# Performance work log

Measured on AMD Instinct MI355X. Metric: run time of the kernel, lower is better.

## Reference

```python
import jax, jax.numpy as jnp
import numpy as np

N_ATOMS = 10000
N_EDGES = 250000
F_DIM = 128
N_RBF = 20
CUTOFF = 5.0
N_INT = 3
EPS = 1e-8


def setup_inputs() -> dict:
    key = jax.random.key(0)
    ks = jax.random.split(key, 16)
    inp = {}
    inp["atomic_numbers"] = jax.random.randint(ks[0], (N_ATOMS,), 1, 101)
    # positions in a 5 Angstrom box so many pairs lie inside the cutoff
    inp["R"] = jax.random.uniform(ks[1], (N_ATOMS, 3), dtype=jnp.float32) * 5.0
    idx_i = jnp.sort(jax.random.randint(ks[2], (N_EDGES,), 0, N_ATOMS))
    # ensure idx_j != idx_i so d_ij > 0
    idx_j = (idx_i + 1 + jax.random.randint(ks[3], (N_EDGES,), 0, N_ATOMS - 1)) % N_ATOMS
    inp["idx_i"] = idx_i
    inp["idx_j"] = idx_j
    inp["offsets"] = jnp.zeros((N_EDGES, 3), dtype=jnp.float32)

    def w(k, shape):
        fan_in = shape[-2]
        return jax.random.normal(k, shape, dtype=jnp.float32) / np.sqrt(fan_in).astype(np.float32)

    inp["emb"] = jax.random.normal(ks[4], (101, F_DIM), dtype=jnp.float32)
    inp["filt_W"] = w(ks[5], (N_RBF, 3 * F_DIM))
    inp["filt_b"] = jax.random.normal(ks[6], (3 * F_DIM,), dtype=jnp.float32) * 0.01
    inp["int_W1"] = w(ks[7], (N_INT, F_DIM, F_DIM))
    inp["int_b1"] = jnp.zeros((N_INT, 1, F_DIM), dtype=jnp.float32)
    inp["int_W2"] = w(ks[8], (N_INT, F_DIM, 3 * F_DIM))
    inp["int_b2"] = jnp.zeros((N_INT, 1, 3 * F_DIM), dtype=jnp.float32)
    inp["mix_Wmu"] = w(ks[9], (N_INT, F_DIM, 2 * F_DIM))
    inp["mix_W1"] = w(ks[10], (N_INT, 2 * F_DIM, F_DIM))
    inp["mix_b1"] = jnp.zeros((N_INT, 1, F_DIM), dtype=jnp.float32)
    inp["mix_W2"] = w(ks[11], (N_INT, F_DIM, 3 * F_DIM))
    inp["mix_b2"] = jnp.zeros((N_INT, 1, 3 * F_DIM), dtype=jnp.float32)
    return inp


def painn_forward(atomic_numbers, idx_i, idx_j, R, offsets, emb, filt_W, filt_b,
                  int_W1, int_b1, int_W2, int_b2,
                  mix_Wmu, mix_W1, mix_b1, mix_W2, mix_b2):
    n_atoms = atomic_numbers.shape[0]
    # geometry
    r_ij = R[idx_j] - R[idx_i] + offsets                      # [E,3]
    d_ij = jnp.linalg.norm(r_ij, axis=1, keepdims=True)       # [E,1]
    dir_ij = r_ij / d_ij                                      # [E,3]
    # Gaussian radial basis + cosine cutoff (schnetpack defaults)
    centers = jnp.linspace(0.0, CUTOFF, N_RBF, dtype=jnp.float32)
    coeff = -0.5 / (centers[1] - centers[0]) ** 2
    phi = jnp.exp(coeff * (d_ij[..., None] - centers) ** 2)   # [E,1,N_RBF]
    fcut = 0.5 * (jnp.cos(d_ij * (jnp.pi / CUTOFF)) + 1.0) * (d_ij < CUTOFF)  # [E,1]
    Wij = (phi @ filt_W + filt_b) * fcut[..., None]           # [E,1,3F] (shared filters)

    q = emb[atomic_numbers][:, None, :]                       # [N,1,F]
    mu = jnp.zeros((n_atoms, 3, F_DIM), dtype=q.dtype)        # [N,3,F]

    for i in range(N_INT):
        # ---- interaction (equivariant message passing) ----
        x = jax.nn.silu(q @ int_W1[i] + int_b1[i]) @ int_W2[i] + int_b2[i]  # [N,1,3F]
        xj = x[idx_j]                                          # [E,1,3F]
        muj = mu[idx_j]                                        # [E,3,F]
        xw = Wij * xj                                          # [E,1,3F]
        dq, dmuR, dmumu = jnp.split(xw, 3, axis=-1)            # each [E,1,F]
        dq = jax.ops.segment_sum(dq, idx_i, num_segments=n_atoms)          # [N,1,F]
        dmu = dmuR * dir_ij[..., None] + dmumu * muj           # [E,3,F]
        dmu = jax.ops.segment_sum(dmu, idx_i, num_segments=n_atoms)        # [N,3,F]
        q = q + dq
        mu = mu + dmu
        # ---- mixing (intra-atomic) ----
        mu_mix = mu @ mix_Wmu[i]                               # [N,3,2F]
        mu_V, mu_W = jnp.split(mu_mix, 2, axis=-1)             # [N,3,F] each
        mu_Vn = jnp.sqrt(jnp.sum(mu_V ** 2, axis=-2, keepdims=True) + EPS)  # [N,1,F]
        ctx = jnp.concatenate([q, mu_Vn], axis=-1)             # [N,1,2F]
        xm = jax.nn.silu(ctx @ mix_W1[i] + mix_b1[i]) @ mix_W2[i] + mix_b2[i]  # [N,1,3F]
        dq_intra, dmu_intra, dqmu_intra = jnp.split(xm, 3, axis=-1)
        dmu_intra = dmu_intra * mu_W                           # [N,3,F]
        dqmu_intra = dqmu_intra * jnp.sum(mu_V * mu_W, axis=1, keepdims=True)  # [N,1,F]
        q = q + dq_intra + dqmu_intra
        mu = mu + dmu_intra

    return q.squeeze(1), mu                                    # [N,F], [N,3,F]


def reference(atomic_numbers, R, idx_i, idx_j, offsets, emb, filt_W, filt_b,
              int_W1, int_b1, int_W2, int_b2,
              mix_Wmu, mix_W1, mix_b1, mix_W2, mix_b2):
    return painn_forward(atomic_numbers, idx_i, idx_j, R, offsets, emb, filt_W, filt_b,
                         int_W1, int_b1, int_W2, int_b2,
                         mix_Wmu, mix_W1, mix_b1, mix_W2, mix_b2)
```

## Files before the change

### kernel.cpp

```cpp
#include <hip/hip_runtime.h>
#include <math.h>

#define NA 10000
#define NE 250000
#define FD 128
#define NRBF 20
#define RCUT 5.0f

typedef _Float16 h16;
typedef __attribute__((ext_vector_type(8))) _Float16 half8;
typedef __attribute__((ext_vector_type(2))) _Float16 half2v;
typedef __attribute__((ext_vector_type(4))) float f32x4;

static __device__ __forceinline__ half8 f32x8_to_h8(const float* p) {
    float4 a = *(const float4*)p;
    float4 b = *(const float4*)(p + 4);
    half8 r;
    r[0] = (h16)a.x; r[1] = (h16)a.y; r[2] = (h16)a.z; r[3] = (h16)a.w;
    r[4] = (h16)b.x; r[5] = (h16)b.y; r[6] = (h16)b.z; r[7] = (h16)b.w;
    return r;
}
static __device__ __forceinline__ float silu(float v) {
    return v / (1.f + expf(-v));
}

__global__ void csr_kernel(const int* __restrict__ idx_i, int* __restrict__ row_start,
                           int* __restrict__ cnt)
{
    int n = blockIdx.x * 256 + threadIdx.x;
    if (n > NA) return;
    int lo = 0, hi = NE;
    while (lo < hi) {
        int mid = (lo + hi) >> 1;
        if (idx_i[mid] < n) lo = mid + 1; else hi = mid;
    }
    row_start[n] = lo;
    if (n < NA) cnt[n] = 0;
}

__global__ __launch_bounds__(256) void setup_kernel(
    const float* __restrict__ R, const int* __restrict__ idx_i,
    const int* __restrict__ idx_j, const float* __restrict__ offsets,
    float* __restrict__ dir, h16* __restrict__ ph, int* __restrict__ jdx,
    const int* __restrict__ row_start, int* __restrict__ cnt,
    const float* __restrict__ int_W1, const float* __restrict__ int_W2,
    const float* __restrict__ mix_Wmu, const float* __restrict__ mix_W1,
    const float* __restrict__ mix_W2,
    h16* __restrict__ W1t, h16* __restrict__ W2t, h16* __restrict__ WmuT,
    h16* __restrict__ mW1t, h16* __restrict__ mW2t,
    const float* __restrict__ filt_W, const float* __restrict__ filt_b,
    h16* __restrict__ fwt)
{
    const int b = blockIdx.x;
    if (b < 977) {
        int e = b * 256 + threadIdx.x;
        if (e >= NE) return;
        int i = idx_i[e], j = idx_j[e];
        float rx = R[j * 3 + 0] - R[i * 3 + 0] + offsets[e * 3 + 0];
        float ry = R[j * 3 + 1] - R[i * 3 + 1] + offsets[e * 3 + 1];
        float rz = R[j * 3 + 2] - R[i * 3 + 2] + offsets[e * 3 + 2];
        float d = sqrtf(rx * rx + ry * ry + rz * rz);
        if (d >= RCUT) return;
        float inv = 1.f / d;
        float fcut = 0.5f * (cosf(d * (3.14159265358979323846f / RCUT)) + 1.f);
        int pos = atomicAdd(&cnt[i], 1);
        int s = row_start[i] + pos;
        *(float4*)&dir[(size_t)s * 4] = make_float4(rx * inv, ry * inv, rz * inv, 0.f);
        jdx[s] = j;
        h16* pp = ph + (size_t)s * 32;
        const float delta = RCUT / 19.f;
        const float coeff = -0.5f / (delta * delta);
#pragma unroll
        for (int r = 0; r < NRBF; ++r) {
            float dc = d - (float)r * delta;
            pp[r] = (h16)(expf(coeff * dc * dc) * fcut);
        }
        pp[20] = (h16)fcut;
#pragma unroll
        for (int r = 21; r < 32; ++r) pp[r] = (h16)0.f;
    } else {
        int idx = (b - 977) * 256 + threadIdx.x;
        if (idx < 49152) {
            int bt = idx >> 14, rem = idx & 16383;
            int nn = rem >> 7, kk = rem & 127;
            W1t[idx] = (h16)int_W1[(size_t)bt * 16384 + kk * 128 + nn];
        } else if ((idx -= 49152) < 147456) {
            int bt = idx / 49152, rem = idx - bt * 49152;
            int nn = rem >> 7, kk = rem & 127;
            W2t[idx] = (h16)int_W2[(size_t)bt * 49152 + kk * 384 + nn];
        } else if ((idx -= 147456) < 98304) {
            int bt = idx >> 15, rem = idx & 32767;
            int nn = rem >> 7, kk = rem & 127;
            WmuT[idx] = (h16)mix_Wmu[(size_t)bt * 32768 + kk * 256 + nn];
        } else if ((idx -= 98304) < 98304) {
            int bt = idx >> 15, rem = idx & 32767;
            int nn = rem >> 8, kk = rem & 255;
            mW1t[idx] = (h16)mix_W1[(size_t)bt * 32768 + kk * 128 + nn];
        } else if ((idx -= 98304) < 147456) {
            int bt = idx / 49152, rem = idx - bt * 49152;
            int nn = rem >> 7, kk = rem & 127;
            mW2t[idx] = (h16)mix_W2[(size_t)bt * 49152 + kk * 384 + nn];
        } else if ((idx -= 147456) < 12288) {
            int nn = idx >> 5, kk = idx & 31;
            float v = 0.f;
            if (kk < 20) v = filt_W[kk * 384 + nn];
            else if (kk == 20) v = filt_b[nn];
            fwt[idx] = (h16)v;
        }
    }
}

__global__ __launch_bounds__(256) void intmlp0_kernel(
    const int* __restrict__ Z, const float* __restrict__ emb, float* __restrict__ q,
    const h16* __restrict__ W1t, const float* __restrict__ b1,
    const h16* __restrict__ W2t, const float* __restrict__ b2, h16* __restrict__ x16)
{
    __shared__ h16 Hs[16 * 136];
    const int tid = threadIdx.x;
    const int wave = tid >> 6, lane = tid & 63;
    const int ar = lane & 15, kg = lane >> 4;
    const size_t row0 = (size_t)blockIdx.x * 16;

    {
        int a = tid >> 4, f0 = (tid & 15) * 8;
        const float* src = emb + (size_t)Z[row0 + a] * 128 + f0;
        float4 v0 = *(const float4*)src;
        float4 v1 = *(const float4*)(src + 4);
        *(float4*)&q[(row0 + a) * 128 + f0] = v0;
        *(float4*)&q[(row0 + a) * 128 + f0 + 4] = v1;
    }
    const int zr = Z[row0 + ar];
    f32x4 a1[2] = {};
    for (int ks = 0; ks < 128; ks += 32) {
        int k = ks + kg * 8;
        half8 af = f32x8_to_h8(emb + (size_t)zr * 128 + k);
#pragma unroll
        for (int tt = 0; tt < 2; ++tt) {
            int t = wave * 2 + tt;
            half8 bf = *(const half8*)&W1t[(size_t)(t * 16 + ar) * 128 + k];
            a1[tt] = __builtin_amdgcn_mfma_f32_16x16x32_f16(af, bf, a1[tt], 0, 0, 0);
        }
    }
#pragma unroll
    for (int tt = 0; tt < 2; ++tt) {
        int col = (wave * 2 + tt) * 16 + ar;
        float bb = b1[col];
#pragma unroll
        for (int r = 0; r < 4; ++r)
            Hs[(kg * 4 + r) * 136 + col] = (h16)silu(a1[tt][r] + bb);
    }
    __syncthreads();
    f32x4 a2[6] = {};
    for (int ks = 0; ks < 128; ks += 32) {
        int k = ks + kg * 8;
        half8 af = *(const half8*)&Hs[ar * 136 + k];
#pragma unroll
        for (int tt = 0; tt < 6; ++tt) {
            int t = wave * 6 + tt;
            half8 bf = *(const half8*)&W2t[(size_t)(t * 16 + ar) * 128 + k];
            a2[tt] = __builtin_amdgcn_mfma_f32_16x16x32_f16(af, bf, a2[tt], 0, 0, 0);
        }
    }
#pragma unroll
    for (int tt = 0; tt < 6; ++tt) {
        int col = (wave * 6 + tt) * 16 + ar;
        float bb = b2[col];
#pragma unroll
        for (int r = 0; r < 4; ++r)
            x16[(row0 + kg * 4 + r) * 384 + col] = (h16)(a2[tt][r] + bb);
    }
}

template<bool HAS_MU>
__global__ __launch_bounds__(128) void edge_kernel(
    const float* __restrict__ dir, const h16* __restrict__ ph,
    const h16* __restrict__ fwt,
    const int* __restrict__ row_start, const int* __restrict__ cnt,
    const int* __restrict__ jdx,
    const h16* __restrict__ x16, const h16* __restrict__ mu16p,
    const float* __restrict__ mup, float* __restrict__ mun,
    h16* __restrict__ mu16n, float* __restrict__ q)
{
    const int n = blockIdx.x, f = threadIdx.x;
    half2v fa[12], fb[12], fc[12];
    {
        const half8* pa = (const half8*)(fwt + (size_t)f * 32);
        const half8* pb = (const half8*)(fwt + (size_t)(128 + f) * 32);
#pragma unroll
        for (int r = 0; r < 3; ++r) {
            *(half8*)&fa[r * 4] = pa[r];
            *(half8*)&fb[r * 4] = pb[r];
        }
        if (HAS_MU) {
            const half8* pc = (const half8*)(fwt + (size_t)(256 + f) * 32);
#pragma unroll
            for (int r = 0; r < 3; ++r)
                *(half8*)&fc[r * 4] = pc[r];
        }
    }
    float accq = 0.f, am0 = 0.f, am1 = 0.f, am2 = 0.f;
    const int e0 = row_start[n], e1 = e0 + cnt[n];
    for (int e = e0; e < e1; ++e) {
        half2v pr[12];
        const h16* pb8 = ph + (size_t)e * 32;
        *(half8*)&pr[0] = *(const half8*)pb8;
        *(half8*)&pr[4] = *(const half8*)(pb8 + 8);
        *(half8*)&pr[8] = *(const half8*)(pb8 + 16);
        half2v A0 = {(h16)0.f, (h16)0.f}, A1 = A0, A2 = A0;
#pragma unroll
        for (int r = 0; r < 11; ++r) {
            A0 = pr[r] * fa[r] + A0;
            A1 = pr[r] * fb[r] + A1;
            if (HAS_MU) A2 = pr[r] * fc[r] + A2;
        }
        float w0 = (float)A0[0] + (float)A0[1];
        float w1 = (float)A1[0] + (float)A1[1];
        int j = jdx[e];
        float4 g = *(const float4*)&dir[(size_t)e * 4];
        const h16* xb = x16 + (size_t)j * 384;
        float x0 = (float)xb[f], x1 = (float)xb[128 + f];
        accq = fmaf(w0, x0, accq);
        float xw1 = w1 * x1;
        if (HAS_MU) {
            float w2 = (float)A2[0] + (float)A2[1];
            float x2 = (float)xb[256 + f];
            float xw2 = w2 * x2;
            const h16* mb = mu16p + (size_t)j * 384;
            am0 += xw1 * g.x + xw2 * (float)mb[f];
            am1 += xw1 * g.y + xw2 * (float)mb[128 + f];
            am2 += xw1 * g.z + xw2 * (float)mb[256 + f];
        } else {
            am0 = fmaf(xw1, g.x, am0);
            am1 = fmaf(xw1, g.y, am1);
            am2 = fmaf(xw1, g.z, am2);
        }
    }
    q[(size_t)n * FD + f] += accq;
    size_t b = (size_t)n * 384;
    float m0 = (HAS_MU ? mup[b + f] : 0.f) + am0;
    float m1 = (HAS_MU ? mup[b + 128 + f] : 0.f) + am1;
    float m2 = (HAS_MU ? mup[b + 256 + f] : 0.f) + am2;
    mun[b + f] = m0; mun[b + 128 + f] = m1; mun[b + 256 + f] = m2;
    mu16n[b + f] = (h16)m0; mu16n[b + 128 + f] = (h16)m1; mu16n[b + 256 + f] = (h16)m2;
}

__global__ __launch_bounds__(256) void mixint_kernel(
    const h16* __restrict__ mu16n, const h16* __restrict__ WmuT,
    const h16* __restrict__ W1t, const float* __restrict__ b1,
    const h16* __restrict__ W2t, const float* __restrict__ b2,
    float* __restrict__ q, float* __restrict__ mu, h16* __restrict__ mu16w,
    const h16* __restrict__ nW1t, const float* __restrict__ nb1,
    const h16* __restrict__ nW2t, const float* __restrict__ nb2,
    h16* __restrict__ x16)
{
    __shared__ h16 MM[48 * 264];
    __shared__ h16 CT[16 * 264];
    __shared__ h16 Hs[16 * 136];
    const int tid = threadIdx.x;
    const int wave = tid >> 6, lane = tid & 63;
    const int ar = lane & 15, kg = lane >> 4;
    const size_t row0 = (size_t)blockIdx.x * 16;

    {
        f32x4 acc[3][4] = {};
        int aloc[3], dloc[3];
#pragma unroll
        for (int rt = 0; rt < 3; ++rt) {
            int rr = rt * 16 + ar;
            aloc[rt] = rr / 3;
            dloc[rt] = rr - 3 * aloc[rt];
        }
        for (int ks = 0; ks < 128; ks += 32) {
            int k = ks + kg * 8;
            half8 afr[3];
#pragma unroll
            for (int rt = 0; rt < 3; ++rt)
                afr[rt] = *(const half8*)&mu16n[(row0 + aloc[rt]) * 384 + dloc[rt] * 128 + k];
#pragma unroll
            for (int ct = 0; ct < 4; ++ct) {
                int cc = wave * 4 + ct;
                half8 bf = *(const half8*)&WmuT[(size_t)(cc * 16 + ar) * 128 + k];
#pragma unroll
                for (int rt = 0; rt < 3; ++rt)
                    acc[rt][ct] = __builtin_amdgcn_mfma_f32_16x16x32_f16(afr[rt], bf, acc[rt][ct], 0, 0, 0);
            }
        }
#pragma unroll
        for (int rt = 0; rt < 3; ++rt)
#pragma unroll
            for (int ct = 0; ct < 4; ++ct) {
                int col = (wave * 4 + ct) * 16 + ar;
#pragma unroll
                for (int r = 0; r < 4; ++r)
                    MM[(rt * 16 + kg * 4 + r) * 264 + col] = (h16)acc[rt][ct][r];
            }
    }
    __syncthreads();

    {
        int a = tid >> 4, fi = (tid & 15) * 8;
        const float* qp = q + (row0 + a) * 128 + fi;
        float4 q0 = *(const float4*)qp;
        float4 q1 = *(const float4*)(qp + 4);
        float qv[8] = {q0.x, q0.y, q0.z, q0.w, q1.x, q1.y, q1.z, q1.w};
#pragma unroll
        for (int jj = 0; jj < 8; ++jj) {
            int ff = fi + jj;
            float v0 = (float)MM[(a * 3 + 0) * 264 + ff];
            float v1 = (float)MM[(a * 3 + 1) * 264 + ff];
            float v2 = (float)MM[(a * 3 + 2) * 264 + ff];
            CT[a * 264 + 128 + ff] = (h16)sqrtf(v0 * v0 + v1 * v1 + v2 * v2 + 1e-8f);
            CT[a * 264 + ff] = (h16)qv[jj];
        }
    }
    __syncthreads();

    {
        f32x4 a1[2] = {};
        for (int ks = 0; ks < 256; ks += 32) {
            int k = ks + kg * 8;
            half8 af = *(const half8*)&CT[ar * 264 + k];
#pragma unroll
            for (int tt = 0; tt < 2; ++tt) {
                int t = wave * 2 + tt;
                half8 bf = *(const half8*)&W1t[(size_t)(t * 16 + ar) * 256 + k];
                a1[tt] = __builtin_amdgcn_mfma_f32_16x16x32_f16(af, bf, a1[tt], 0, 0, 0);
            }
        }
#pragma unroll
        for (int tt = 0; tt < 2; ++tt) {
            int col = (wave * 2 + tt) * 16 + ar;
            float bb = b1[col];
#pragma unroll
            for (int r = 0; r < 4; ++r)
                Hs[(kg * 4 + r) * 136 + col] = (h16)silu(a1[tt][r] + bb);
        }
    }
    __syncthreads();

    f32x4 aq[2] = {}, am[2] = {}, ag[2] = {};
    for (int ks = 0; ks < 128; ks += 32) {
        int k = ks + kg * 8;
        half8 af = *(const half8*)&Hs[ar * 136 + k];
#pragma unroll
        for (int p = 0; p < 2; ++p) {
            int t = wave * 2 + p;
            half8 bq = *(const half8*)&W2t[(size_t)(t * 16 + ar) * 128 + k];
            aq[p] = __builtin_amdgcn_mfma_f32_16x16x32_f16(af, bq, aq[p], 0, 0, 0);
            half8 bm = *(const half8*)&W2t[(size_t)((8 + t) * 16 + ar) * 128 + k];
            am[p] = __builtin_amdgcn_mfma_f32_16x16x32_f16(af, bm, am[p], 0, 0, 0);
            half8 bg = *(const half8*)&W2t[(size_t)((16 + t) * 16 + ar) * 128 + k];
            ag[p] = __builtin_amdgcn_mfma_f32_16x16x32_f16(af, bg, ag[p], 0, 0, 0);
        }
    }

#pragma unroll
    for (int p = 0; p < 2; ++p) {
        int f = (wave * 2 + p) * 16 + ar;
        float bdq = b2[f], bdm = b2[128 + f], bdg = b2[256 + f];
#pragma unroll
        for (int r = 0; r < 4; ++r) {
            int aL = kg * 4 + r;
            size_t n = row0 + aL;
            float dq  = aq[p][r] + bdq;
            float dm  = am[p][r] + bdm;
            float dqm = ag[p][r] + bdg;
            float v0 = (float)MM[(aL * 3 + 0) * 264 + f], w0 = (float)MM[(aL * 3 + 0) * 264 + 128 + f];
            float v1 = (float)MM[(aL * 3 + 1) * 264 + f], w1 = (float)MM[(aL * 3 + 1) * 264 + 128 + f];
            float v2 = (float)MM[(aL * 3 + 2) * 264 + f], w2 = (float)MM[(aL * 3 + 2) * 264 + 128 + f];
            float sv = v0 * w0 + v1 * w1 + v2 * w2;
            float qn = q[n * 128 + f] + dq + dqm * sv;
            q[n * 128 + f] = qn;
            CT[aL * 264 + f] = (h16)qn;
            size_t b = n * 384 + f;
            float m0 = mu[b] + dm * w0;
            float m1 = mu[b + 128] + dm * w1;
            float m2 = mu[b + 256] + dm * w2;
            mu[b] = m0; mu[b + 128] = m1; mu[b + 256] = m2;
            mu16w[b] = (h16)m0; mu16w[b + 128] = (h16)m1; mu16w[b + 256] = (h16)m2;
        }
    }
    if (!nW1t) return;
    __syncthreads();

    {
        f32x4 a1[2] = {};
        for (int ks = 0; ks < 128; ks += 32) {
            int k = ks + kg * 8;
            half8 af = *(const half8*)&CT[ar * 264 + k];
#pragma unroll
            for (int tt = 0; tt < 2; ++tt) {
                int t = wave * 2 + tt;
                half8 bf = *(const half8*)&nW1t[(size_t)(t * 16 + ar) * 128 + k];
                a1[tt] = __builtin_amdgcn_mfma_f32_16x16x32_f16(af, bf, a1[tt], 0, 0, 0);
            }
        }
#pragma unroll
        for (int tt = 0; tt < 2; ++tt) {
            int col = (wave * 2 + tt) * 16 + ar;
            float bb = nb1[col];
#pragma unroll
            for (int r = 0; r < 4; ++r)
                Hs[(kg * 4 + r) * 136 + col] = (h16)silu(a1[tt][r] + bb);
        }
        __syncthreads();
        f32x4 a2[6] = {};
        for (int ks = 0; ks < 128; ks += 32) {
            int k = ks + kg * 8;
            half8 af = *(const half8*)&Hs[ar * 136 + k];
#pragma unroll
            for (int tt = 0; tt < 6; ++tt) {
                int t = wave * 6 + tt;
                half8 bf = *(const half8*)&nW2t[(size_t)(t * 16 + ar) * 128 + k];
                a2[tt] = __builtin_amdgcn_mfma_f32_16x16x32_f16(af, bf, a2[tt], 0, 0, 0);
            }
        }
#pragma unroll
        for (int tt = 0; tt < 6; ++tt) {
            int col = (wave * 6 + tt) * 16 + ar;
            float bb = nb2[col];
#pragma unroll
            for (int r = 0; r < 4; ++r)
                x16[(row0 + kg * 4 + r) * 384 + col] = (h16)(a2[tt][r] + bb);
        }
    }
}

extern "C" void kernel_launch(void* const* d_in, const int* in_sizes, int n_in,
                              void* d_out, int out_size, void* d_ws, size_t ws_size,
                              hipStream_t stream)
{
    const int*   Z       = (const int*)d_in[0];
    const float* R       = (const float*)d_in[1];
    const int*   idx_i   = (const int*)d_in[2];
    const int*   idx_j   = (const int*)d_in[3];
    const float* offsets = (const float*)d_in[4];
    const float* emb     = (const float*)d_in[5];
    const float* filt_W  = (const float*)d_in[6];
    const float* filt_b  = (const float*)d_in[7];
    const float* int_W1  = (const float*)d_in[8];
    const float* int_b1  = (const float*)d_in[9];
    const float* int_W2  = (const float*)d_in[10];
    const float* int_b2  = (const float*)d_in[11];
    const float* mix_Wmu = (const float*)d_in[12];
    const float* mix_W1  = (const float*)d_in[13];
    const float* mix_b1  = (const float*)d_in[14];
    const float* mix_W2  = (const float*)d_in[15];
    const float* mix_b2  = (const float*)d_in[16];

    float* q_out  = (float*)d_out;
    float* mu_out = (float*)d_out + (size_t)NA * FD;

    char* base = (char*)d_ws;
    size_t o = 0;
    auto alloc = [&](size_t bytes) -> void* {
        void* p = base + o;
        o += (bytes + 255) & ~(size_t)255;
        return p;
    };
    float* dir    = (float*)alloc((size_t)NE * 4 * 4);
    h16*   ph     = (h16*)alloc((size_t)NE * 32 * 2);
    int*   jdx    = (int*)alloc((size_t)NE * 4);
    h16*   x16    = (h16*)alloc((size_t)NA * 384 * 2);
    h16*   mu16a  = (h16*)alloc((size_t)NA * 384 * 2);
    h16*   mu16b  = (h16*)alloc((size_t)NA * 384 * 2);
    float* mu_ws  = (float*)alloc((size_t)NA * 384 * 4);
    h16*   W1t    = (h16*)alloc((size_t)3 * 128 * 128 * 2);
    h16*   W2t    = (h16*)alloc((size_t)3 * 384 * 128 * 2);
    h16*   WmuT   = (h16*)alloc((size_t)3 * 256 * 128 * 2);
    h16*   mW1t   = (h16*)alloc((size_t)3 * 128 * 256 * 2);
    h16*   mW2t   = (h16*)alloc((size_t)3 * 384 * 128 * 2);
    h16*   fwt    = (h16*)alloc((size_t)384 * 32 * 2);
    int*   row_st = (int*)alloc((size_t)(NA + 1) * 4);
    int*   cnt    = (int*)alloc((size_t)NA * 4);

    csr_kernel<<<(NA + 256) / 256, 256, 0, stream>>>(idx_i, row_st, cnt);
    setup_kernel<<<3137, 256, 0, stream>>>(R, idx_i, idx_j, offsets, dir, ph, jdx,
                                           row_st, cnt,
                                           int_W1, int_W2, mix_Wmu, mix_W1, mix_W2,
                                           W1t, W2t, WmuT, mW1t, mW2t,
                                           filt_W, filt_b, fwt);

    intmlp0_kernel<<<NA / 16, 256, 0, stream>>>(Z, emb, q_out,
                                                W1t, int_b1, W2t, int_b2, x16);
    edge_kernel<false><<<NA, 128, 0, stream>>>(dir, ph, fwt, row_st, cnt, jdx,
                                               x16, nullptr, nullptr, mu_out, mu16b, q_out);
    mixint_kernel<<<NA / 16, 256, 0, stream>>>(
        mu16b, WmuT, mW1t, mix_b1, mW2t, mix_b2, q_out, mu_out, mu16b,
        W1t + 16384, int_b1 + 128, W2t + 49152, int_b2 + 384, x16);

    edge_kernel<true><<<NA, 128, 0, stream>>>(dir, ph, fwt, row_st, cnt, jdx,
                                              x16, mu16b, mu_out, mu_ws, mu16a, q_out);
    mixint_kernel<<<NA / 16, 256, 0, stream>>>(
        mu16a, WmuT + 32768, mW1t + 32768, mix_b1 + 128, mW2t + 49152, mix_b2 + 384,
        q_out, mu_ws, mu16a,
        W1t + 32768, int_b1 + 256, W2t + 98304, int_b2 + 768, x16);

    edge_kernel<true><<<NA, 128, 0, stream>>>(dir, ph, fwt, row_st, cnt, jdx,
                                              x16, mu16a, mu_ws, mu_out, mu16b, q_out);
    mixint_kernel<<<NA / 16, 256, 0, stream>>>(
        mu16b, WmuT + 65536, mW1t + 65536, mix_b1 + 256, mW2t + 98304, mix_b2 + 768,
        q_out, mu_out, mu16b,
        nullptr, nullptr, nullptr, nullptr, nullptr);
}
```

Before: 478.4 us.

## Fold CSR row-start search into setup kernel and halve mixint block size

Removes the separate csr_kernel: each edge thread binary-searches its own row start, extra blocks in setup_kernel write row_start, and cnt is zeroed with hipMemsetAsync. This cuts one kernel launch and its serialization. mixint_kernel now handles 8 atoms per block instead of 16, doubling the grid to gain parallelism, at the cost of wasted MFMA lanes, padded rows and more redundant weight loads per atom. The per-edge binary search adds a lot of global reads to setup.

After: 568.8 us. +18.9%, slower.

```diff
diff --git a/kernel.cpp b/kernel.cpp
--- a/kernel.cpp
+++ b/kernel.cpp
@@ -6,6 +6,7 @@
 #define FD 128
 #define NRBF 20
 #define RCUT 5.0f
+#define AB 8
 
 typedef _Float16 h16;
 typedef __attribute__((ext_vector_type(8))) _Float16 half8;
@@ -24,25 +25,11 @@
     return v / (1.f + expf(-v));
 }
 
-__global__ void csr_kernel(const int* __restrict__ idx_i, int* __restrict__ row_start,
-                           int* __restrict__ cnt)
-{
-    int n = blockIdx.x * 256 + threadIdx.x;
-    if (n > NA) return;
-    int lo = 0, hi = NE;
-    while (lo < hi) {
-        int mid = (lo + hi) >> 1;
-        if (idx_i[mid] < n) lo = mid + 1; else hi = mid;
-    }
-    row_start[n] = lo;
-    if (n < NA) cnt[n] = 0;
-}
-
 __global__ __launch_bounds__(256) void setup_kernel(
     const float* __restrict__ R, const int* __restrict__ idx_i,
     const int* __restrict__ idx_j, const float* __restrict__ offsets,
     float* __restrict__ dir, h16* __restrict__ ph, int* __restrict__ jdx,
-    const int* __restrict__ row_start, int* __restrict__ cnt,
+    int* __restrict__ row_start, int* __restrict__ cnt,
     const float* __restrict__ int_W1, const float* __restrict__ int_W2,
     const float* __restrict__ mix_Wmu, const float* __restrict__ mix_W1,
     const float* __restrict__ mix_W2,
@@ -63,8 +50,13 @@
         if (d >= RCUT) return;
         float inv = 1.f / d;
         float fcut = 0.5f * (cosf(d * (3.14159265358979323846f / RCUT)) + 1.f);
+        int lo = 0, hi = NE;
+        while (lo < hi) {
+            int mid = (lo + hi) >> 1;
+            if (idx_i[mid] < i) lo = mid + 1; else hi = mid;
+        }
         int pos = atomicAdd(&cnt[i], 1);
-        int s = row_start[i] + pos;
+        int s = lo + pos;
         *(float4*)&dir[(size_t)s * 4] = make_float4(rx * inv, ry * inv, rz * inv, 0.f);
         jdx[s] = j;
         h16* pp = ph + (size_t)s * 32;
@@ -78,7 +70,7 @@
         pp[20] = (h16)fcut;
 #pragma unroll
         for (int r = 21; r < 32; ++r) pp[r] = (h16)0.f;
-    } else {
+    } else if (b < 3137) {
         int idx = (b - 977) * 256 + threadIdx.x;
         if (idx < 49152) {
             int bt = idx >> 14, rem = idx & 16383;
@@ -107,6 +99,15 @@
             else if (kk == 20) v = filt_b[nn];
             fwt[idx] = (h16)v;
         }
+    } else {
+        int n = (b - 3137) * 256 + threadIdx.x;
+        if (n > NA) return;
+        int lo = 0, hi = NE;
+        while (lo < hi) {
+            int mid = (lo + hi) >> 1;
+            if (idx_i[mid] < n) lo = mid + 1; else hi = mid;
+        }
+        row_start[n] = lo;
     }
 }
 
@@ -253,40 +254,40 @@
     const h16* __restrict__ nW2t, const float* __restrict__ nb2,
     h16* __restrict__ x16)
 {
-    __shared__ h16 MM[48 * 264];
+    __shared__ h16 MM[32 * 264];
     __shared__ h16 CT[16 * 264];
     __shared__ h16 Hs[16 * 136];
     const int tid = threadIdx.x;
     const int wave = tid >> 6, lane = tid & 63;
     const int ar = lane & 15, kg = lane >> 4;
-    const size_t row0 = (size_t)blockIdx.x * 16;
+    const size_t row0 = (size_t)blockIdx.x * AB;
 
     {
-        f32x4 acc[3][4] = {};
-        int aloc[3], dloc[3];
-#pragma unroll
-        for (int rt = 0; rt < 3; ++rt) {
+        f32x4 acc[2][4] = {};
+        int aloc[2], dloc[2];
+#pragma unroll
+        for (int rt = 0; rt < 2; ++rt) {
             int rr = rt * 16 + ar;
-            aloc[rt] = rr / 3;
-            dloc[rt] = rr - 3 * aloc[rt];
+            if (rr < 3 * AB) { aloc[rt] = rr / 3; dloc[rt] = rr - 3 * (rr / 3); }
+            else             { aloc[rt] = AB - 1; dloc[rt] = 2; }
         }
         for (int ks = 0; ks < 128; ks += 32) {
             int k = ks + kg * 8;
-            half8 afr[3];
-#pragma unroll
-            for (int rt = 0; rt < 3; ++rt)
+            half8 afr[2];
+#pragma unroll
+            for (int rt = 0; rt < 2; ++rt)
                 afr[rt] = *(const half8*)&mu16n[(row0 + aloc[rt]) * 384 + dloc[rt] * 128 + k];
 #pragma unroll
             for (int ct = 0; ct < 4; ++ct) {
                 int cc = wave * 4 + ct;
                 half8 bf = *(const half8*)&WmuT[(size_t)(cc * 16 + ar) * 128 + k];
 #pragma unroll
-                for (int rt = 0; rt < 3; ++rt)
+                for (int rt = 0; rt < 2; ++rt)
                     acc[rt][ct] = __builtin_amdgcn_mfma_f32_16x16x32_f16(afr[rt], bf, acc[rt][ct], 0, 0, 0);
             }
         }
 #pragma unroll
-        for (int rt = 0; rt < 3; ++rt)
+        for (int rt = 0; rt < 2; ++rt)
 #pragma unroll
             for (int ct = 0; ct < 4; ++ct) {
                 int col = (wave * 4 + ct) * 16 + ar;
@@ -299,16 +300,17 @@
 
     {
         int a = tid >> 4, fi = (tid & 15) * 8;
-        const float* qp = q + (row0 + a) * 128 + fi;
+        int aa = a < AB ? a : AB - 1;
+        const float* qp = q + (row0 + aa) * 128 + fi;
         float4 q0 = *(const float4*)qp;
         float4 q1 = *(const float4*)(qp + 4);
         float qv[8] = {q0.x, q0.y, q0.z, q0.w, q1.x, q1.y, q1.z, q1.w};
 #pragma unroll
         for (int jj = 0; jj < 8; ++jj) {
             int ff = fi + jj;
-            float v0 = (float)MM[(a * 3 + 0) * 264 + ff];
-            float v1 = (float)MM[(a * 3 + 1) * 264 + ff];
-            float v2 = (float)MM[(a * 3 + 2) * 264 + ff];
+            float v0 = (float)MM[(aa * 3 + 0) * 264 + ff];
+            float v1 = (float)MM[(aa * 3 + 1) * 264 + ff];
+            float v2 = (float)MM[(aa * 3 + 2) * 264 + ff];
             CT[a * 264 + 128 + ff] = (h16)sqrtf(v0 * v0 + v1 * v1 + v2 * v2 + 1e-8f);
             CT[a * 264 + ff] = (h16)qv[jj];
         }
@@ -361,23 +363,25 @@
 #pragma unroll
         for (int r = 0; r < 4; ++r) {
             int aL = kg * 4 + r;
-            size_t n = row0 + aL;
-            float dq  = aq[p][r] + bdq;
-            float dm  = am[p][r] + bdm;
-            float dqm = ag[p][r] + bdg;
-            float v0 = (float)MM[(aL * 3 + 0) * 264 + f], w0 = (float)MM[(aL * 3 + 0) * 264 + 128 + f];
-            float v1 = (float)MM[(aL * 3 + 1) * 264 + f], w1 = (float)MM[(aL * 3 + 1) * 264 + 128 + f];
-            float v2 = (float)MM[(aL * 3 + 2) * 264 + f], w2 = (float)MM[(aL * 3 + 2) * 264 + 128 + f];
-            float sv = v0 * w0 + v1 * w1 + v2 * w2;
-            float qn = q[n * 128 + f] + dq + dqm * sv;
-            q[n * 128 + f] = qn;
-            CT[aL * 264 + f] = (h16)qn;
-            size_t b = n * 384 + f;
-            float m0 = mu[b] + dm * w0;
-            float m1 = mu[b + 128] + dm * w1;
-            float m2 = mu[b + 256] + dm * w2;
-            mu[b] = m0; mu[b + 128] = m1; mu[b + 256] = m2;
-            mu16w[b] = (h16)m0; mu16w[b + 128] = (h16)m1; mu16w[b + 256] = (h16)m2;
+            if (aL < AB) {
+                size_t n = row0 + aL;
+                float dq  = aq[p][r] + bdq;
+                float dm  = am[p][r] + bdm;
+                float dqm = ag[p][r] + bdg;
+                float v0 = (float)MM[(aL * 3 + 0) * 264 + f], w0 = (float)MM[(aL * 3 + 0) * 264 + 128 + f];
+                float v1 = (float)MM[(aL * 3 + 1) * 264 + f], w1 = (float)MM[(aL * 3 + 1) * 264 + 128 + f];
+                float v2 = (float)MM[(aL * 3 + 2) * 264 + f], w2 = (float)MM[(aL * 3 + 2) * 264 + 128 + f];
+                float sv = v0 * w0 + v1 * w1 + v2 * w2;
+                float qn = q[n * 128 + f] + dq + dqm * sv;
+                q[n * 128 + f] = qn;
+                CT[aL * 264 + f] = (h16)qn;
+                size_t b = n * 384 + f;
+                float m0 = mu[b] + dm * w0;
+                float m1 = mu[b + 128] + dm * w1;
+                float m2 = mu[b + 256] + dm * w2;
+                mu[b] = m0; mu[b + 128] = m1; mu[b + 256] = m2;
+                mu16w[b] = (h16)m0; mu16w[b + 128] = (h16)m1; mu16w[b + 256] = (h16)m2;
+            }
         }
     }
     if (!nW1t) return;
@@ -420,8 +424,11 @@
             int col = (wave * 6 + tt) * 16 + ar;
             float bb = nb2[col];
 #pragma unroll
-            for (int r = 0; r < 4; ++r)
-                x16[(row0 + kg * 4 + r) * 384 + col] = (h16)(a2[tt][r] + bb);
+            for (int r = 0; r < 4; ++r) {
+                int aL = kg * 4 + r;
+                if (aL < AB)
+                    x16[(row0 + aL) * 384 + col] = (h16)(a2[tt][r] + bb);
+            }
         }
     }
 }
@@ -474,8 +481,8 @@
     int*   row_st = (int*)alloc((size_t)(NA + 1) * 4);
     int*   cnt    = (int*)alloc((size_t)NA * 4);
 
-    csr_kernel<<<(NA + 256) / 256, 256, 0, stream>>>(idx_i, row_st, cnt);
-    setup_kernel<<<3137, 256, 0, stream>>>(R, idx_i, idx_j, offsets, dir, ph, jdx,
+    hipMemsetAsync(cnt, 0, (size_t)NA * 4, stream);
+    setup_kernel<<<3177, 256, 0, stream>>>(R, idx_i, idx_j, offsets, dir, ph, jdx,
                                            row_st, cnt,
                                            int_W1, int_W2, mix_Wmu, mix_W1, mix_W2,
                                            W1t, W2t, WmuT, mW1t, mW2t,
@@ -485,20 +492,20 @@
                                                 W1t, int_b1, W2t, int_b2, x16);
     edge_kernel<false><<<NA, 128, 0, stream>>>(dir, ph, fwt, row_st, cnt, jdx,
                                                x16, nullptr, nullptr, mu_out, mu16b, q_out);
-    mixint_kernel<<<NA / 16, 256, 0, stream>>>(
+    mixint_kernel<<<NA / AB, 256, 0, stream>>>(
         mu16b, WmuT, mW1t, mix_b1, mW2t, mix_b2, q_out, mu_out, mu16b,
         W1t + 16384, int_b1 + 128, W2t + 49152, int_b2 + 384, x16);
 
     edge_kernel<true><<<NA, 128, 0, stream>>>(dir, ph, fwt, row_st, cnt, jdx,
                                               x16, mu16b, mu_out, mu_ws, mu16a, q_out);
-    mixint_kernel<<<NA / 16, 256, 0, stream>>>(
+    mixint_kernel<<<NA / AB, 256, 0, stream>>>(
         mu16a, WmuT + 32768, mW1t + 32768, mix_b1 + 128, mW2t + 49152, mix_b2 + 384,
         q_out, mu_ws, mu16a,
         W1t + 32768, int_b1 + 256, W2t + 98304, int_b2 + 768, x16);
 
     edge_kernel<true><<<NA, 128, 0, stream>>>(dir, ph, fwt, row_st, cnt, jdx,
                                               x16, mu16a, mu_ws, mu_out, mu16b, q_out);
-    mixint_kernel<<<NA / 16, 256, 0, stream>>>(
+    mixint_kernel<<<NA / AB, 256, 0, stream>>>(
         mu16b, WmuT + 65536, mW1t + 65536, mix_b1 + 256, mW2t + 98304, mix_b2 + 768,
         q_out, mu_out, mu16b,
         nullptr, nullptr, nullptr, nullptr, nullptr);
```
